# Performance work log

Measured on AMD Instinct MI355X. Metric: run time of the kernel, lower is better.

## Reference

```python
import jax, jax.numpy as jnp
import numpy as np

# tcnn-style multiresolution hash grid config (Instant-NGP defaults)
L = 16            # n_levels
F = 2             # n_features_per_level
T = 1 << 19       # hashmap size per level (log2_hashmap_size = 19)
BASE = 16.0       # base_resolution
SCALE = 1.38      # per_level_scale
N = 131072        # number of query points (pixels/rays)
HIDDEN = 64
OUT = 9

PRIMES = jnp.array([1, 2654435761, 805459861, 3674653429], dtype=jnp.uint32)
# 16 corner offsets of the 4-D hypercube, shape [16, 4]
OFFS = ((jnp.arange(16, dtype=jnp.uint32)[:, None] >> jnp.arange(4, dtype=jnp.uint32)[None, :]) & jnp.uint32(1))


def hash_encode(x, table):
    """x: [N,4] in [0,1); table: [L*T, F]. Returns [N, L*F]."""
    res = jnp.floor(BASE * jnp.power(jnp.float32(SCALE), jnp.arange(L, dtype=jnp.float32)))  # [L]
    pos = x[None, :, :] * res[:, None, None]            # [L,N,4]
    p0f = jnp.floor(pos)
    frac = pos - p0f                                    # [L,N,4]
    p0 = p0f.astype(jnp.uint32)
    corners = p0[:, :, None, :] + OFFS[None, None]      # [L,N,16,4]
    h = corners * PRIMES                                # wrapping uint32 mul
    h = h[..., 0] ^ h[..., 1] ^ h[..., 2] ^ h[..., 3]   # [L,N,16]
    level_off = (jnp.arange(L, dtype=jnp.uint32) * jnp.uint32(T))[:, None, None]
    idx = (h & jnp.uint32(T - 1)) + level_off           # [L,N,16]
    feats = table[idx]                                  # [L,N,16,F]
    # 4-linear interpolation weights: prod over dims of frac or (1-frac)
    w = jnp.prod(jnp.where(OFFS[None, None].astype(bool),
                           frac[:, :, None, :], 1.0 - frac[:, :, None, :]), axis=-1)  # [L,N,16]
    enc = jnp.einsum('lnc,lncf->lnf', w, feats)         # [L,N,F]
    return enc.transpose(1, 0, 2).reshape(x.shape[0], L * F)


def setup_inputs() -> dict:
    key = jax.random.key(0)
    k0, k1, k2, k3, k4, k5 = jax.random.split(key, 6)
    return {
        "img_pixel_indices": jax.random.uniform(k0, (N, 2), jnp.float32),
        "pose_extended": jax.random.uniform(k1, (N, 2), jnp.float32),
        "hash_table": jax.random.uniform(k2, (L * T, F), jnp.float32, -1e-4, 1e-4),
        "W1": jax.random.normal(k3, (L * F, HIDDEN), jnp.float32) * np.float32(1.0 / np.sqrt(L * F)),
        "W2": jax.random.normal(k4, (HIDDEN, HIDDEN), jnp.float32) * np.float32(1.0 / np.sqrt(HIDDEN)),
        "W3": jax.random.normal(k5, (HIDDEN, OUT), jnp.float32) * np.float32(1.0 / np.sqrt(HIDDEN)),
    }


def reference(img_pixel_indices, pose_extended, hash_table, W1, W2, W3):
    # cat((img_pixel_indices, pose_extended), dim=1) -> 4-D encoder input
    x = jnp.concatenate([img_pixel_indices, pose_extended], axis=1)  # [N,4]
    enc = hash_encode(x, hash_table)                                 # [N, L*F]
    h = jax.nn.relu(enc @ W1)
    h = jax.nn.relu(h @ W2)
    return h @ W3                                                    # [N, 9]
```

## Files before the change

### kernel.cpp

```cpp
#include <hip/hip_runtime.h>
#include <stdint.h>

#define LVLS 16
#define TSZ (1u << 19)
#define PR1 2654435761u
#define PR2 805459861u
#define PR3 3674653429u

__global__ __launch_bounds__(256, 8) void encode_kernel(
    const float* __restrict__ img, const float* __restrict__ pose,
    const float* __restrict__ table, float* __restrict__ encbuf,
    int npts, int Bper)
{
    const int bid = blockIdx.x;
    const int grp = 8 * Bper;
    const int level = (bid % 8) + 8 * (bid / grp);
    const int within = (bid % grp) / 8;

    const int idx = within * 256 + threadIdx.x;
    const int p = idx >> 1;
    const int s = idx & 1;
    if (p >= npts) return;

    const float2 xi = ((const float2*)img)[p];
    const float2 xp = ((const float2*)pose)[p];

    constexpr float resv[LVLS] = {16.f, 22.f, 30.f, 42.f, 58.f, 80.f, 110.f, 152.f,
                                  210.f, 290.f, 400.f, 553.f, 763.f, 1053.f, 1453.f, 2005.f};
    const float rr = resv[level];

    const float s0 = xi.x * rr, s1 = xi.y * rr, s2 = xp.x * rr, s3 = xp.y * rr;
    const float p0f = floorf(s0), p1f = floorf(s1), p2f = floorf(s2), p3f = floorf(s3);
    const float f0 = s0 - p0f, f1 = s1 - p1f, f2 = s2 - p2f, f3 = s3 - p3f;
    const uint32_t q0 = (uint32_t)p0f, q1 = (uint32_t)p1f,
                   q2 = (uint32_t)p2f, q3 = (uint32_t)p3f;

    const uint32_t b0  = q0 + (uint32_t)s;
    const uint32_t h1a = q1 * PR1, h1b = h1a + PR1;
    const uint32_t h2a = q2 * PR2, h2b = h2a + PR2;
    const uint32_t h3a = q3 * PR3, h3b = h3a + PR3;
    const uint32_t loff = (uint32_t)level * TSZ;

    const float2* __restrict__ tab2 = (const float2*)table;

    float2 f[8];
    #pragma unroll
    for (int c = 0; c < 8; ++c) {
        const uint32_t h = b0 ^ ((c & 1) ? h1b : h1a)
                              ^ ((c & 2) ? h2b : h2a)
                              ^ ((c & 4) ? h3b : h3a);
        f[c] = tab2[(h & (TSZ - 1u)) + loff];
    }

    const float w0 = s ? f0 : 1.f - f0;
    const float w1a = 1.f - f1, w2a = 1.f - f2, w3a = 1.f - f3;

    float e0 = 0.f, e1 = 0.f;
    #pragma unroll
    for (int c = 0; c < 8; ++c) {
        const float w = w0 * ((c & 1) ? f1 : w1a)
                           * ((c & 2) ? f2 : w2a)
                           * ((c & 4) ? f3 : w3a);
        e0 = fmaf(w, f[c].x, e0);
        e1 = fmaf(w, f[c].y, e1);
    }

    e0 += __shfl_xor(e0, 1);
    e1 += __shfl_xor(e1, 1);

    if (s == 0)
        ((float2*)encbuf)[(size_t)level * npts + p] = make_float2(e0, e1);
}

__global__ __launch_bounds__(256, 4) void mlp_kernel(
    const float* __restrict__ encbuf, const float* __restrict__ W1,
    const float* __restrict__ W2, const float* __restrict__ W3,
    float* __restrict__ out, int npts)
{
    __shared__ __align__(16) char ldsbuf[64 * 128 * 4];
    float (*h1S)[128]   = (float (*)[128])ldsbuf;
    float (*oS)[128][9] = (float (*)[128][9])ldsbuf;

    const int lane = threadIdx.x & 63;
    const int w    = __builtin_amdgcn_readfirstlane(threadIdx.x >> 6);
    const int pA   = blockIdx.x * 128 + lane;
    const int pB   = pA + 64;

    const float* __restrict__ W1w = W1 + 16 * w;
    float hA[16], hB[16];
    #pragma unroll
    for (int j = 0; j < 16; ++j) { hA[j] = 0.f; hB[j] = 0.f; }
    const float2* e2 = (const float2*)encbuf;
    #pragma unroll
    for (int l = 0; l < LVLS; ++l) {
        const float2 eA = e2[(size_t)l * npts + pA];
        const float2 eB = e2[(size_t)l * npts + pB];
        #pragma unroll
        for (int j = 0; j < 16; ++j) {
            const float w0 = W1w[(2 * l) * 64 + j];
            const float w1 = W1w[(2 * l + 1) * 64 + j];
            hA[j] = fmaf(eA.x, w0, hA[j]); hA[j] = fmaf(eA.y, w1, hA[j]);
            hB[j] = fmaf(eB.x, w0, hB[j]); hB[j] = fmaf(eB.y, w1, hB[j]);
        }
    }
    #pragma unroll
    for (int j = 0; j < 16; ++j) {
        h1S[16 * w + j][lane]      = fmaxf(hA[j], 0.f);
        h1S[16 * w + j][lane + 64] = fmaxf(hB[j], 0.f);
    }
    __syncthreads();

    const float* __restrict__ W2w = W2 + 16 * w;
    float gA[16], gB[16];
    #pragma unroll
    for (int j = 0; j < 16; ++j) { gA[j] = 0.f; gB[j] = 0.f; }
    #pragma unroll
    for (int i = 0; i < 64; ++i) {
        const float eA = h1S[i][lane];
        const float eB = h1S[i][lane + 64];
        #pragma unroll
        for (int j = 0; j < 16; ++j) {
            const float wv = W2w[i * 64 + j];
            gA[j] = fmaf(eA, wv, gA[j]);
            gB[j] = fmaf(eB, wv, gB[j]);
        }
    }
    #pragma unroll
    for (int j = 0; j < 16; ++j) { gA[j] = fmaxf(gA[j], 0.f); gB[j] = fmaxf(gB[j], 0.f); }

    const float* __restrict__ W3w = W3 + (16 * w) * 9;
    float oA[9], oB[9];
    #pragma unroll
    for (int k = 0; k < 9; ++k) { oA[k] = 0.f; oB[k] = 0.f; }
    #pragma unroll
    for (int j = 0; j < 16; ++j) {
        #pragma unroll
        for (int k = 0; k < 9; ++k) {
            const float wv = W3w[j * 9 + k];
            oA[k] = fmaf(gA[j], wv, oA[k]);
            oB[k] = fmaf(gB[j], wv, oB[k]);
        }
    }

    __syncthreads();

    if (w > 0) {
        #pragma unroll
        for (int k = 0; k < 9; ++k) {
            oS[w - 1][lane][k]      = oA[k];
            oS[w - 1][lane + 64][k] = oB[k];
        }
    }
    __syncthreads();
    if (w == 0) {
        float* dstA = out + (size_t)9 * pA;
        float* dstB = out + (size_t)9 * pB;
        #pragma unroll
        for (int k = 0; k < 9; ++k)
            dstA[k] = oA[k] + oS[0][lane][k] + oS[1][lane][k] + oS[2][lane][k];
        #pragma unroll
        for (int k = 0; k < 9; ++k)
            dstB[k] = oB[k] + oS[0][lane + 64][k] + oS[1][lane + 64][k] + oS[2][lane + 64][k];
    }
}

__global__ __launch_bounds__(256) void hashgrid_mlp_kernel(
    const float* __restrict__ img, const float* __restrict__ pose,
    const float* __restrict__ table, const float* __restrict__ W1,
    const float* __restrict__ W2, const float* __restrict__ W3,
    float* __restrict__ out)
{
    const int n = blockIdx.x * 256 + threadIdx.x;

    const float x0 = img[2 * n], x1 = img[2 * n + 1];
    const float x2 = pose[2 * n], x3 = pose[2 * n + 1];

    const float resv[LVLS] = {16.f, 22.f, 30.f, 42.f, 58.f, 80.f, 110.f, 152.f,
                              210.f, 290.f, 400.f, 553.f, 763.f, 1053.f, 1453.f, 2005.f};

    const float2* __restrict__ tab2 = (const float2*)table;

    float enc[32];

    #pragma unroll
    for (int l = 0; l < LVLS; ++l) {
        const float r = resv[l];
        const float s0 = x0 * r, s1 = x1 * r, s2 = x2 * r, s3 = x3 * r;
        const float p0 = floorf(s0), p1 = floorf(s1), p2 = floorf(s2), p3 = floorf(s3);
        const float f0 = s0 - p0, f1 = s1 - p1, f2 = s2 - p2, f3 = s3 - p3;
        const uint32_t q0 = (uint32_t)p0, q1 = (uint32_t)p1,
                       q2 = (uint32_t)p2, q3 = (uint32_t)p3;

        const uint32_t h1a = q1 * PR1, h1b = h1a + PR1;
        const uint32_t h2a = q2 * PR2, h2b = h2a + PR2;
        const uint32_t h3a = q3 * PR3, h3b = h3a + PR3;
        const float w0a = 1.f - f0, w1a = 1.f - f1, w2a = 1.f - f2, w3a = 1.f - f3;

        float2 feat[16];
        #pragma unroll
        for (int c = 0; c < 16; ++c) {
            const uint32_t h = (q0 + (c & 1))
                             ^ ((c & 2) ? h1b : h1a)
                             ^ ((c & 4) ? h2b : h2a)
                             ^ ((c & 8) ? h3b : h3a);
            const uint32_t idx = (h & (TSZ - 1u)) + (uint32_t)l * TSZ;
            feat[c] = tab2[idx];
        }

        float e0 = 0.f, e1 = 0.f;
        #pragma unroll
        for (int c = 0; c < 16; ++c) {
            const float w = ((c & 1) ? f0 : w0a) * ((c & 2) ? f1 : w1a)
                          * ((c & 4) ? f2 : w2a) * ((c & 8) ? f3 : w3a);
            e0 = fmaf(w, feat[c].x, e0);
            e1 = fmaf(w, feat[c].y, e1);
        }
        enc[2 * l]     = e0;
        enc[2 * l + 1] = e1;
    }

    float h1[64];
    #pragma unroll
    for (int j = 0; j < 64; ++j) h1[j] = 0.f;
    #pragma unroll
    for (int i = 0; i < 32; ++i) {
        const float e = enc[i];
        #pragma unroll
        for (int j = 0; j < 64; ++j) h1[j] = fmaf(e, W1[i * 64 + j], h1[j]);
    }
    #pragma unroll
    for (int j = 0; j < 64; ++j) h1[j] = fmaxf(h1[j], 0.f);

    float h2[64];
    #pragma unroll
    for (int j = 0; j < 64; ++j) h2[j] = 0.f;
    #pragma unroll
    for (int i = 0; i < 64; ++i) {
        const float e = h1[i];
        #pragma unroll
        for (int j = 0; j < 64; ++j) h2[j] = fmaf(e, W2[i * 64 + j], h2[j]);
    }
    #pragma unroll
    for (int j = 0; j < 64; ++j) h2[j] = fmaxf(h2[j], 0.f);

    float o[9];
    #pragma unroll
    for (int j = 0; j < 9; ++j) o[j] = 0.f;
    #pragma unroll
    for (int i = 0; i < 64; ++i) {
        const float e = h2[i];
        #pragma unroll
        for (int j = 0; j < 9; ++j) o[j] = fmaf(e, W3[i * 9 + j], o[j]);
    }
    #pragma unroll
    for (int j = 0; j < 9; ++j) out[9 * n + j] = o[j];
}

extern "C" void kernel_launch(void* const* d_in, const int* in_sizes, int n_in,
                              void* d_out, int out_size, void* d_ws, size_t ws_size,
                              hipStream_t stream) {
    const float* img   = (const float*)d_in[0];
    const float* pose  = (const float*)d_in[1];
    const float* table = (const float*)d_in[2];
    const float* W1    = (const float*)d_in[3];
    const float* W2    = (const float*)d_in[4];
    const float* W3    = (const float*)d_in[5];
    float* out = (float*)d_out;

    const int n = in_sizes[0] / 2;
    const size_t need = (size_t)n * 32 * sizeof(float);

    if (ws_size >= need && (n % 128) == 0 && ((n * 2) % 256) == 0) {
        float* encbuf = (float*)d_ws;
        const int Bper = (n * 2) / 256;
        hipLaunchKernelGGL(encode_kernel, dim3(Bper * LVLS), dim3(256), 0, stream,
                           img, pose, table, encbuf, n, Bper);
        hipLaunchKernelGGL(mlp_kernel, dim3(n / 128), dim3(256), 0, stream,
                           encbuf, W1, W2, W3, out, n);
    } else {
        hipLaunchKernelGGL(hashgrid_mlp_kernel, dim3((n + 255) / 256), dim3(256), 0, stream,
                           img, pose, table, W1, W2, W3, out);
    }
}
```

Measured before the change: 120.6 us.

## Compute full MLP per thread in registers, drop LDS split across waves

The MLP kernel no longer splits the hidden units across four waves with shared-memory exchange and a cross-wave reduction. Each thread now processes one point end to end, holding 64 hidden activations in registers, and reads the weights as uniform (scalar) loads. This removes the LDS traffic and block barriers. In exchange it raises register pressure, with launch bounds lowered to 2 blocks, and uses one point per thread instead of two per lane, which reduces weight reuse per load and may lower occupancy.

```diff
diff --git a/kernel.cpp b/kernel.cpp
--- a/kernel.cpp
+++ b/kernel.cpp
@@ -72,96 +72,56 @@
         ((float2*)encbuf)[(size_t)level * npts + p] = make_float2(e0, e1);
 }
 
-__global__ __launch_bounds__(256, 4) void mlp_kernel(
+__global__ __launch_bounds__(256, 2) void mlp_kernel(
     const float* __restrict__ encbuf, const float* __restrict__ W1,
     const float* __restrict__ W2, const float* __restrict__ W3,
     float* __restrict__ out, int npts)
 {
-    __shared__ __align__(16) char ldsbuf[64 * 128 * 4];
-    float (*h1S)[128]   = (float (*)[128])ldsbuf;
-    float (*oS)[128][9] = (float (*)[128][9])ldsbuf;
-
-    const int lane = threadIdx.x & 63;
-    const int w    = __builtin_amdgcn_readfirstlane(threadIdx.x >> 6);
-    const int pA   = blockIdx.x * 128 + lane;
-    const int pB   = pA + 64;
-
-    const float* __restrict__ W1w = W1 + 16 * w;
-    float hA[16], hB[16];
-    #pragma unroll
-    for (int j = 0; j < 16; ++j) { hA[j] = 0.f; hB[j] = 0.f; }
-    const float2* e2 = (const float2*)encbuf;
+    const int p = blockIdx.x * 256 + threadIdx.x;
+    if (p >= npts) return;
+
+    const float2* __restrict__ e2 = (const float2*)encbuf;
+
+    float h[64];
+    #pragma unroll
+    for (int j = 0; j < 64; ++j) h[j] = 0.f;
     #pragma unroll
     for (int l = 0; l < LVLS; ++l) {
-        const float2 eA = e2[(size_t)l * npts + pA];
-        const float2 eB = e2[(size_t)l * npts + pB];
-        #pragma unroll
-        for (int j = 0; j < 16; ++j) {
-            const float w0 = W1w[(2 * l) * 64 + j];
-            const float w1 = W1w[(2 * l + 1) * 64 + j];
-            hA[j] = fmaf(eA.x, w0, hA[j]); hA[j] = fmaf(eA.y, w1, hA[j]);
-            hB[j] = fmaf(eB.x, w0, hB[j]); hB[j] = fmaf(eB.y, w1, hB[j]);
+        const float2 e = e2[(size_t)l * npts + p];
+        #pragma unroll
+        for (int j = 0; j < 64; ++j) {
+            h[j] = fmaf(e.x, W1[(2 * l) * 64 + j], h[j]);
+            h[j] = fmaf(e.y, W1[(2 * l + 1) * 64 + j], h[j]);
         }
     }
     #pragma unroll
-    for (int j = 0; j < 16; ++j) {
-        h1S[16 * w + j][lane]      = fmaxf(hA[j], 0.f);
-        h1S[16 * w + j][lane + 64] = fmaxf(hB[j], 0.f);
-    }
-    __syncthreads();
-
-    const float* __restrict__ W2w = W2 + 16 * w;
-    float gA[16], gB[16];
-    #pragma unroll
-    for (int j = 0; j < 16; ++j) { gA[j] = 0.f; gB[j] = 0.f; }
+    for (int j = 0; j < 64; ++j) h[j] = fmaxf(h[j], 0.f);
+
+    float g[64];
+    #pragma unroll
+    for (int j = 0; j < 64; ++j) g[j] = 0.f;
     #pragma unroll
     for (int i = 0; i < 64; ++i) {
-        const float eA = h1S[i][lane];
-        const float eB = h1S[i][lane + 64];
-        #pragma unroll
-        for (int j = 0; j < 16; ++j) {
-            const float wv = W2w[i * 64 + j];
-            gA[j] = fmaf(eA, wv, gA[j]);
-            gB[j] = fmaf(eB, wv, gB[j]);
-        }
-    }
-    #pragma unroll
-    for (int j = 0; j < 16; ++j) { gA[j] = fmaxf(gA[j], 0.f); gB[j] = fmaxf(gB[j], 0.f); }
-
-    const float* __restrict__ W3w = W3 + (16 * w) * 9;
-    float oA[9], oB[9];
-    #pragma unroll
-    for (int k = 0; k < 9; ++k) { oA[k] = 0.f; oB[k] = 0.f; }
-    #pragma unroll
-    for (int j = 0; j < 16; ++j) {
-        #pragma unroll
-        for (int k = 0; k < 9; ++k) {
-            const float wv = W3w[j * 9 + k];
-            oA[k] = fmaf(gA[j], wv, oA[k]);
-            oB[k] = fmaf(gB[j], wv, oB[k]);
-        }
-    }
-
-    __syncthreads();
-
-    if (w > 0) {
-        #pragma unroll
-        for (int k = 0; k < 9; ++k) {
-            oS[w - 1][lane][k]      = oA[k];
-            oS[w - 1][lane + 64][k] = oB[k];
-        }
-    }
-    __syncthreads();
-    if (w == 0) {
-        float* dstA = out + (size_t)9 * pA;
-        float* dstB = out + (size_t)9 * pB;
+        const float hi = h[i];
+        #pragma unroll
+        for (int j = 0; j < 64; ++j)
+            g[j] = fmaf(hi, W2[i * 64 + j], g[j]);
+    }
+
+    float o[9];
+    #pragma unroll
+    for (int k = 0; k < 9; ++k) o[k] = 0.f;
+    #pragma unroll
+    for (int j = 0; j < 64; ++j) {
+        const float gj = fmaxf(g[j], 0.f);
         #pragma unroll
         for (int k = 0; k < 9; ++k)
-            dstA[k] = oA[k] + oS[0][lane][k] + oS[1][lane][k] + oS[2][lane][k];
-        #pragma unroll
-        for (int k = 0; k < 9; ++k)
-            dstB[k] = oB[k] + oS[0][lane + 64][k] + oS[1][lane + 64][k] + oS[2][lane + 64][k];
-    }
+            o[k] = fmaf(gj, W3[j * 9 + k], o[k]);
+    }
+
+    float* dst = out + (size_t)9 * p;
+    #pragma unroll
+    for (int k = 0; k < 9; ++k) dst[k] = o[k];
 }
 
 __global__ __launch_bounds__(256) void hashgrid_mlp_kernel(
@@ -275,7 +235,7 @@
         const int Bper = (n * 2) / 256;
         hipLaunchKernelGGL(encode_kernel, dim3(Bper * LVLS), dim3(256), 0, stream,
                            img, pose, table, encbuf, n, Bper);
-        hipLaunchKernelGGL(mlp_kernel, dim3(n / 128), dim3(256), 0, stream,
+        hipLaunchKernelGGL(mlp_kernel, dim3((n + 255) / 256), dim3(256), 0, stream,
                            encbuf, W1, W2, W3, out, n);
     } else {
         hipLaunchKernelGGL(hashgrid_mlp_kernel, dim3((n + 255) / 256), dim3(256), 0, stream,
```

Result: slower. 142.1 us (+17.8%).
